# Kernel tuning notes

Hardware: AMD Instinct MI355X
Metric: run time of the kernel (lower is better)

Reference implementation:

```python
import jax, jax.numpy as jnp
import numpy as np

B, S, H = 1, 2048, 1024      # batch, seq, hidden_size
E, I, K = 32, 768, 4         # num_experts, moe_intermediate_size, top_k
NORM_TOPK = True


def setup_inputs() -> dict:
    key = jax.random.key(0)
    k0, k1, k2, k3, k4 = jax.random.split(key, 5)
    sc = 0.02  # typical init std
    return {
        "hidden_states": jax.random.normal(k0, (B, S, H), dtype=jnp.float32),
        "router_w": jax.random.normal(k1, (E, H), dtype=jnp.float32) * sc,
        "gate_w":   jax.random.normal(k2, (E, I, H), dtype=jnp.float32) * sc,
        "up_w":     jax.random.normal(k3, (E, I, H), dtype=jnp.float32) * sc,
        "down_w":   jax.random.normal(k4, (E, H, I), dtype=jnp.float32) * sc,
    }


def _moe(hidden_states, router_w, gate_w, up_w, down_w):
    b, s, h = hidden_states.shape
    x = hidden_states.reshape(-1, h)                       # [T, H]
    # --- router: linear -> fp32 softmax -> top-k -> renorm ---
    logits = x @ router_w.T                                # [T, E]
    probs = jax.nn.softmax(logits.astype(jnp.float32), axis=-1)
    vals, idx = jax.lax.top_k(probs, K)                    # [T, K]
    if NORM_TOPK:
        vals = vals / jnp.sum(vals, axis=-1, keepdims=True)
    vals = vals.astype(x.dtype)
    # dense combine weights [T, E]: zero for unselected experts
    combine = jnp.sum(jax.nn.one_hot(idx, probs.shape[-1], dtype=x.dtype)
                      * vals[..., None], axis=1)           # [T, E]
    # --- per-expert gated-SiLU MLP, weighted combine (scan over experts) ---
    def step(acc, ws):
        wg, wu, wd, we = ws                                # [I,H],[I,H],[H,I],[T]
        hidden = jax.nn.silu(x @ wg.T) * (x @ wu.T)        # [T, I]
        return acc + we[:, None] * (hidden @ wd.T), None
    acc0 = jnp.zeros_like(x)
    out, _ = jax.lax.scan(step, acc0, (gate_w, up_w, down_w, combine.T))
    return out.reshape(b, s, h)


def reference(hidden_states, router_w, gate_w, up_w, down_w):
    return _moe(hidden_states, router_w, gate_w, up_w, down_w)
```

## Files before the change

kernel.cpp:

```cpp
#include <hip/hip_runtime.h>
#include <hip/hip_bf16.h>

typedef __attribute__((ext_vector_type(8))) short short8;
typedef __attribute__((ext_vector_type(4))) float f32x4;

#define T_TOK 2048
#define H_DIM 1024
#define E_NUM 32
#define I_DIM 768
#define TOPK  4
#define NPAIR (T_TOK*TOPK)

#define OFF_IDX     0
#define OFF_TKW     (32*1024)
#define OFF_COUNTS  (64*1024)
#define OFF_OFFSETS (65*1024)
#define OFF_CURSORS (66*1024)
#define OFF_PERM    (68*1024)
#define OFF_PAIRW   (100*1024)
#define OFF_POS     (132*1024)
#define OFF_XBF     (1024*1024)
#define OFF_H       (6*1024*1024)
#define OFF_Y       (20*1024*1024)

__device__ __forceinline__ unsigned short f2bf(float f) {
    __hip_bfloat16 b = __float2bfloat16(f);
    unsigned short u;
    __builtin_memcpy(&u, &b, 2);
    return u;
}
__device__ __forceinline__ unsigned int pk2(float lo, float hi) {
    return (unsigned int)f2bf(lo) | ((unsigned int)f2bf(hi) << 16);
}

__global__ __launch_bounds__(256)
void k_xcvt(const float* __restrict__ x, unsigned short* __restrict__ xbf)
{
    int g = blockIdx.x * 256 + threadIdx.x;
    const float4* p = (const float4*)(x + (size_t)g * 8);
    float4 a = p[0], b = p[1];
    uint4 o = { pk2(a.x,a.y), pk2(a.z,a.w), pk2(b.x,b.y), pk2(b.z,b.w) };
    *(uint4*)(xbf + (size_t)g * 8) = o;
}

__global__ __launch_bounds__(64)
void k_router(const float* __restrict__ x, const float* __restrict__ rw,
              int* __restrict__ idx, float* __restrict__ tkw, int* __restrict__ counts)
{
    int t = blockIdx.x;
    int lane = threadIdx.x;
    const float4* xr = (const float4*)(x + (size_t)t * H_DIM);
    float4 xv[4];
#pragma unroll
    for (int m = 0; m < 4; ++m) xv[m] = xr[m * 64 + lane];

    __shared__ float logits[E_NUM];
    for (int e = 0; e < E_NUM; ++e) {
        const float4* wr = (const float4*)(rw + (size_t)e * H_DIM);
        float acc = 0.f;
#pragma unroll
        for (int m = 0; m < 4; ++m) {
            float4 wv = wr[m * 64 + lane];
            acc += xv[m].x * wv.x + xv[m].y * wv.y + xv[m].z * wv.z + xv[m].w * wv.w;
        }
#pragma unroll
        for (int s = 32; s > 0; s >>= 1) acc += __shfl_xor(acc, s);
        if (lane == 0) logits[e] = acc;
    }
    __syncthreads();
    if (lane == 0) {
        float m = -1e30f;
        for (int e = 0; e < E_NUM; ++e) m = fmaxf(m, logits[e]);
        for (int e = 0; e < E_NUM; ++e) logits[e] = expf(logits[e] - m);
        float vals[TOPK]; int ids[TOPK]; float s = 0.f;
        for (int k = 0; k < TOPK; ++k) {
            float bv = -1.f; int be = 0;
            for (int e = 0; e < E_NUM; ++e)
                if (logits[e] > bv) { bv = logits[e]; be = e; }
            vals[k] = bv; ids[k] = be; logits[be] = -2.f; s += bv;
        }
        float invs = 1.f / s;
        for (int k = 0; k < TOPK; ++k) {
            idx[t * TOPK + k] = ids[k];
            tkw[t * TOPK + k] = vals[k] * invs;
            atomicAdd(&counts[ids[k]], 1);
        }
    }
}

__global__ void k_scan(const int* __restrict__ counts, int* __restrict__ offsets,
                       int* __restrict__ cursors)
{
    if (threadIdx.x == 0) {
        int acc = 0;
        for (int e = 0; e < E_NUM; ++e) { offsets[e] = acc; cursors[e] = acc; acc += counts[e]; }
        offsets[E_NUM] = acc;
    }
}

__global__ __launch_bounds__(256)
void k_scatter(const int* __restrict__ idx, const float* __restrict__ tkw,
               int* __restrict__ cursors, int* __restrict__ perm,
               float* __restrict__ pairw, int* __restrict__ pos)
{
    int g = blockIdx.x * 256 + threadIdx.x;
    if (g >= NPAIR) return;
    int e = idx[g];
    int p = atomicAdd(&cursors[e], 1);
    perm[p] = g >> 2;
    pairw[p] = tkw[g];
    pos[g] = p;
}

#define GU_BN 64
#define GU_BM 256
#define GU_BK 64
#define PAD   72

__global__ __launch_bounds__(256, 2)
void k_gateup(const unsigned short* __restrict__ xbf, const float* __restrict__ gw,
              const float* __restrict__ uw, const int* __restrict__ offsets,
              const int* __restrict__ perm, unsigned short* __restrict__ h)
{
    int e  = blockIdx.z;
    int r0 = offsets[e], r1 = offsets[e + 1];
    int row0 = r0 + blockIdx.y * GU_BM;
    if (row0 >= r1) return;
    int nrows = min(GU_BM, r1 - row0);
    int ib = blockIdx.x * GU_BN;

    __shared__ __align__(16) unsigned short As[GU_BM * PAD];
    __shared__ __align__(16) unsigned short Bgs[GU_BN * PAD];
    __shared__ __align__(16) unsigned short Bus[GU_BN * PAD];
    __shared__ int rtok[GU_BM];

    int tid = threadIdx.x;
    rtok[tid] = perm[min(row0 + tid, r1 - 1)];

    const float* wgb = gw + ((size_t)e * I_DIM + ib) * H_DIM;
    const float* wub = uw + ((size_t)e * I_DIM + ib) * H_DIM;

    int w = tid >> 6;
    int lane = tid & 63;
    int l15 = lane & 15, lhi = lane >> 4;

    f32x4 accg[4][4], accu[4][4];
#pragma unroll
    for (int a = 0; a < 4; ++a)
#pragma unroll
        for (int b = 0; b < 4; ++b) { accg[a][b] = 0.f; accu[a][b] = 0.f; }

    for (int kb = 0; kb < H_DIM; kb += GU_BK) {
        __syncthreads();
#pragma unroll
        for (int p = 0; p < 8; ++p) {
            int q = tid + p * 256;
            int row = q >> 3, kg = q & 7;
            uint4 v = *(const uint4*)(xbf + (size_t)rtok[row] * H_DIM + kb + kg * 8);
            *(uint4*)&As[row * PAD + kg * 8] = v;
        }
#pragma unroll
        for (int p = 0; p < 2; ++p) {
            int q = tid + p * 256;
            int row = q >> 3, kg = q & 7;
            const float* sg = wgb + (size_t)row * H_DIM + kb + kg * 8;
            float4 a0 = *(const float4*)sg, a1 = *(const float4*)(sg + 4);
            uint4 vg = { pk2(a0.x,a0.y), pk2(a0.z,a0.w), pk2(a1.x,a1.y), pk2(a1.z,a1.w) };
            *(uint4*)&Bgs[row * PAD + kg * 8] = vg;
            const float* su = wub + (size_t)row * H_DIM + kb + kg * 8;
            float4 b0 = *(const float4*)su, b1 = *(const float4*)(su + 4);
            uint4 vu = { pk2(b0.x,b0.y), pk2(b0.z,b0.w), pk2(b1.x,b1.y), pk2(b1.z,b1.w) };
            *(uint4*)&Bus[row * PAD + kg * 8] = vu;
        }
        __syncthreads();
#pragma unroll
        for (int kk = 0; kk < 2; ++kk) {
            short8 av[4], bgv[4], buv[4];
            int ko = kk * 32 + lhi * 8;
#pragma unroll
            for (int f = 0; f < 4; ++f) {
                av[f]  = *(const short8*)&As[(w * 64 + f * 16 + l15) * PAD + ko];
                bgv[f] = *(const short8*)&Bgs[(f * 16 + l15) * PAD + ko];
                buv[f] = *(const short8*)&Bus[(f * 16 + l15) * PAD + ko];
            }
#pragma unroll
            for (int fm = 0; fm < 4; ++fm)
#pragma unroll
                for (int fn = 0; fn < 4; ++fn) {
                    accg[fm][fn] = __builtin_amdgcn_mfma_f32_16x16x32_bf16(av[fm], bgv[fn], accg[fm][fn], 0, 0, 0);
                    accu[fm][fn] = __builtin_amdgcn_mfma_f32_16x16x32_bf16(av[fm], buv[fn], accu[fm][fn], 0, 0, 0);
                }
        }
    }
#pragma unroll
    for (int fm = 0; fm < 4; ++fm) {
#pragma unroll
        for (int j = 0; j < 4; ++j) {
            int r = w * 64 + fm * 16 + lhi * 4 + j;
            if (r < nrows) {
                size_t orow = (size_t)(row0 + r) * I_DIM + ib + l15;
#pragma unroll
                for (int fn = 0; fn < 4; ++fn) {
                    float g = accg[fm][fn][j];
                    float u = accu[fm][fn][j];
                    float hv = (g / (1.f + __expf(-g))) * u;
                    h[orow + fn * 16] = f2bf(hv);
                }
            }
        }
    }
}

#define DN_BN 64
#define DN_BM 256
#define DN_BK 64

__global__ __launch_bounds__(256, 2)
void k_down(const float* __restrict__ dw, const int* __restrict__ offsets,
            const float* __restrict__ pairw, const unsigned short* __restrict__ h,
            float* __restrict__ y)
{
    int e  = blockIdx.z;
    int r0 = offsets[e], r1 = offsets[e + 1];
    int row0 = r0 + blockIdx.y * DN_BM;
    if (row0 >= r1) return;
    int nrows = min(DN_BM, r1 - row0);
    int cb = blockIdx.x * DN_BN;

    __shared__ __align__(16) unsigned short As[DN_BM * PAD];
    __shared__ __align__(16) unsigned short Bs[DN_BN * PAD];
    __shared__ float pw[DN_BM];

    int tid = threadIdx.x;
    pw[tid] = pairw[min(row0 + tid, r1 - 1)];

    const float* wdb = dw + ((size_t)e * H_DIM + cb) * I_DIM;
    int w = tid >> 6, lane = tid & 63;
    int l15 = lane & 15, lhi = lane >> 4;

    f32x4 acc[4][4];
#pragma unroll
    for (int a = 0; a < 4; ++a)
#pragma unroll
        for (int b = 0; b < 4; ++b) acc[a][b] = 0.f;

    for (int kb = 0; kb < I_DIM; kb += DN_BK) {
        __syncthreads();
#pragma unroll
        for (int p = 0; p < 8; ++p) {
            int q = tid + p * 256;
            int row = q >> 3, kg = q & 7;
            int rr = min(row0 + row, r1 - 1);
            uint4 v = *(const uint4*)(h + (size_t)rr * I_DIM + kb + kg * 8);
            *(uint4*)&As[row * PAD + kg * 8] = v;
        }
#pragma unroll
        for (int p = 0; p < 2; ++p) {
            int q = tid + p * 256;
            int row = q >> 3, kg = q & 7;
            const float* sd = wdb + (size_t)row * I_DIM + kb + kg * 8;
            float4 a0 = *(const float4*)sd, a1 = *(const float4*)(sd + 4);
            uint4 vd = { pk2(a0.x,a0.y), pk2(a0.z,a0.w), pk2(a1.x,a1.y), pk2(a1.z,a1.w) };
            *(uint4*)&Bs[row * PAD + kg * 8] = vd;
        }
        __syncthreads();
#pragma unroll
        for (int kk = 0; kk < 2; ++kk) {
            short8 av[4], bv[4];
            int ko = kk * 32 + lhi * 8;
#pragma unroll
            for (int f = 0; f < 4; ++f) {
                av[f] = *(const short8*)&As[(w * 64 + f * 16 + l15) * PAD + ko];
                bv[f] = *(const short8*)&Bs[(f * 16 + l15) * PAD + ko];
            }
#pragma unroll
            for (int fm = 0; fm < 4; ++fm)
#pragma unroll
                for (int fn = 0; fn < 4; ++fn)
                    acc[fm][fn] = __builtin_amdgcn_mfma_f32_16x16x32_bf16(av[fm], bv[fn], acc[fm][fn], 0, 0, 0);
        }
    }
#pragma unroll
    for (int fm = 0; fm < 4; ++fm) {
#pragma unroll
        for (int j = 0; j < 4; ++j) {
            int r = w * 64 + fm * 16 + lhi * 4 + j;
            if (r < nrows) {
                float s = pw[r];
                size_t orow = (size_t)(row0 + r) * H_DIM + cb + l15;
#pragma unroll
                for (int fn = 0; fn < 4; ++fn)
                    y[orow + fn * 16] = s * acc[fm][fn][j];
            }
        }
    }
}

__global__ __launch_bounds__(256)
void k_combine(const float* __restrict__ y, const int* __restrict__ pos,
               float* __restrict__ out)
{
    int g = blockIdx.x * 256 + threadIdx.x;
    int t = g >> 10;
    int hc = g & 1023;
    const int* pp = pos + t * TOPK;
    float s = y[(size_t)pp[0] * H_DIM + hc] + y[(size_t)pp[1] * H_DIM + hc]
            + y[(size_t)pp[2] * H_DIM + hc] + y[(size_t)pp[3] * H_DIM + hc];
    out[g] = s;
}

extern "C" void kernel_launch(void* const* d_in, const int* in_sizes, int n_in,
                              void* d_out, int out_size, void* d_ws, size_t ws_size,
                              hipStream_t stream)
{
    const float* x  = (const float*)d_in[0];
    const float* rw = (const float*)d_in[1];
    const float* gw = (const float*)d_in[2];
    const float* uw = (const float*)d_in[3];
    const float* dw = (const float*)d_in[4];
    float* out = (float*)d_out;

    char* ws = (char*)d_ws;
    int*   idx     = (int*)  (ws + OFF_IDX);
    float* tkw     = (float*)(ws + OFF_TKW);
    int*   counts  = (int*)  (ws + OFF_COUNTS);
    int*   offsets = (int*)  (ws + OFF_OFFSETS);
    int*   cursors = (int*)  (ws + OFF_CURSORS);
    int*   perm    = (int*)  (ws + OFF_PERM);
    float* pairw   = (float*)(ws + OFF_PAIRW);
    int*   pos     = (int*)  (ws + OFF_POS);
    unsigned short* xbf = (unsigned short*)(ws + OFF_XBF);
    unsigned short* h   = (unsigned short*)(ws + OFF_H);
    float* y            = (float*)(ws + OFF_Y);

    hipMemsetAsync(counts, 0, E_NUM * sizeof(int), stream);

    k_xcvt<<<T_TOK * H_DIM / (256 * 8), 256, 0, stream>>>(x, xbf);
    k_router<<<T_TOK, 64, 0, stream>>>(x, rw, idx, tkw, counts);
    k_scan<<<1, 64, 0, stream>>>(counts, offsets, cursors);
    k_scatter<<<(NPAIR + 255) / 256, 256, 0, stream>>>(idx, tkw, cursors, perm, pairw, pos);

    dim3 g3(I_DIM / GU_BN, NPAIR / GU_BM, E_NUM);
    k_gateup<<<g3, 256, 0, stream>>>(xbf, gw, uw, offsets, perm, h);

    dim3 g4(H_DIM / DN_BN, NPAIR / DN_BM, E_NUM);
    k_down<<<g4, 256, 0, stream>>>(dw, offsets, pairw, h, y);

    k_combine<<<T_TOK * H_DIM / 256, 256, 0, stream>>>(y, pos, out);
}
```

Measured before the change: 479.2 us.

## Register-prefetch next K tile in gate/up and down GEMMs

Both expert GEMM kernels now load the next K tile from global memory into registers while MFMAs run on the current shared-memory tile, then write those registers to LDS after a barrier. Token and row indices are hoisted into per-thread registers so they are not recomputed each iteration. This is meant to hide global load latency behind compute. The cost is higher register pressure: roughly 32 VGPRs for the A prefetch plus weight staging, on top of 128 accumulator values in gate/up. That could hurt occupancy under launch_bounds(256,2) or cause spills.

```diff
diff --git a/kernel.cpp b/kernel.cpp
--- a/kernel.cpp
+++ b/kernel.cpp
@@ -116,6 +116,7 @@
 #define GU_BM 256
 #define GU_BK 64
 #define PAD   72
+#define GU_NT (H_DIM / GU_BK)
 
 __global__ __launch_bounds__(256, 2)
 void k_gateup(const unsigned short* __restrict__ xbf, const float* __restrict__ gw,
@@ -136,6 +137,12 @@
 
     int tid = threadIdx.x;
     rtok[tid] = perm[min(row0 + tid, r1 - 1)];
+    __syncthreads();
+
+    int mytok[8];
+#pragma unroll
+    for (int p = 0; p < 8; ++p) mytok[p] = rtok[(tid + p * 256) >> 3];
+    int akg = tid & 7;
 
     const float* wgb = gw + ((size_t)e * I_DIM + ib) * H_DIM;
     const float* wub = uw + ((size_t)e * I_DIM + ib) * H_DIM;
@@ -150,29 +157,44 @@
 #pragma unroll
         for (int b = 0; b < 4; ++b) { accg[a][b] = 0.f; accu[a][b] = 0.f; }
 
-    for (int kb = 0; kb < H_DIM; kb += GU_BK) {
+    uint4 pa[8];
+    float4 pg0[2], pg1[2], pu0[2], pu1[2];
+
+#define GU_LOAD(KB) do {                                                          \
+    _Pragma("unroll")                                                             \
+    for (int p = 0; p < 8; ++p)                                                   \
+        pa[p] = *(const uint4*)(xbf + (size_t)mytok[p] * H_DIM + (KB) + akg * 8); \
+    _Pragma("unroll")                                                             \
+    for (int it = 0; it < 2; ++it) {                                              \
+        int q = tid + it * 256; int brow = q >> 3, bkg = q & 7;                   \
+        const float* sg = wgb + (size_t)brow * H_DIM + (KB) + bkg * 8;            \
+        pg0[it] = *(const float4*)sg; pg1[it] = *(const float4*)(sg + 4);         \
+        const float* su = wub + (size_t)brow * H_DIM + (KB) + bkg * 8;            \
+        pu0[it] = *(const float4*)su; pu1[it] = *(const float4*)(su + 4);         \
+    } } while (0)
+
+#define GU_WRITE() do {                                                           \
+    _Pragma("unroll")                                                             \
+    for (int p = 0; p < 8; ++p) {                                                 \
+        int arow = (tid + p * 256) >> 3;                                          \
+        *(uint4*)&As[arow * PAD + akg * 8] = pa[p];                               \
+    }                                                                             \
+    _Pragma("unroll")                                                             \
+    for (int it = 0; it < 2; ++it) {                                              \
+        int q = tid + it * 256; int brow = q >> 3, bkg = q & 7;                   \
+        uint4 vg = { pk2(pg0[it].x,pg0[it].y), pk2(pg0[it].z,pg0[it].w),          \
+                     pk2(pg1[it].x,pg1[it].y), pk2(pg1[it].z,pg1[it].w) };        \
+        *(uint4*)&Bgs[brow * PAD + bkg * 8] = vg;                                 \
+        uint4 vu = { pk2(pu0[it].x,pu0[it].y), pk2(pu0[it].z,pu0[it].w),          \
+                     pk2(pu1[it].x,pu1[it].y), pk2(pu1[it].z,pu1[it].w) };        \
+        *(uint4*)&Bus[brow * PAD + bkg * 8] = vu;                                 \
+    } } while (0)
+
+    GU_LOAD(0);
+    for (int kt = 0; kt < GU_NT; ++kt) {
+        GU_WRITE();
         __syncthreads();
-#pragma unroll
-        for (int p = 0; p < 8; ++p) {
-            int q = tid + p * 256;
-            int row = q >> 3, kg = q & 7;
-            uint4 v = *(const uint4*)(xbf + (size_t)rtok[row] * H_DIM + kb + kg * 8);
-            *(uint4*)&As[row * PAD + kg * 8] = v;
-        }
-#pragma unroll
-        for (int p = 0; p < 2; ++p) {
-            int q = tid + p * 256;
-            int row = q >> 3, kg = q & 7;
-            const float* sg = wgb + (size_t)row * H_DIM + kb + kg * 8;
-            float4 a0 = *(const float4*)sg, a1 = *(const float4*)(sg + 4);
-            uint4 vg = { pk2(a0.x,a0.y), pk2(a0.z,a0.w), pk2(a1.x,a1.y), pk2(a1.z,a1.w) };
-            *(uint4*)&Bgs[row * PAD + kg * 8] = vg;
-            const float* su = wub + (size_t)row * H_DIM + kb + kg * 8;
-            float4 b0 = *(const float4*)su, b1 = *(const float4*)(su + 4);
-            uint4 vu = { pk2(b0.x,b0.y), pk2(b0.z,b0.w), pk2(b1.x,b1.y), pk2(b1.z,b1.w) };
-            *(uint4*)&Bus[row * PAD + kg * 8] = vu;
-        }
-        __syncthreads();
+        if (kt + 1 < GU_NT) GU_LOAD((kt + 1) * GU_BK);
 #pragma unroll
         for (int kk = 0; kk < 2; ++kk) {
             short8 av[4], bgv[4], buv[4];
@@ -191,6 +213,7 @@
                     accu[fm][fn] = __builtin_amdgcn_mfma_f32_16x16x32_bf16(av[fm], buv[fn], accu[fm][fn], 0, 0, 0);
                 }
         }
+        __syncthreads();
     }
 #pragma unroll
     for (int fm = 0; fm < 4; ++fm) {
@@ -214,6 +237,7 @@
 #define DN_BN 64
 #define DN_BM 256
 #define DN_BK 64
+#define DN_NT (I_DIM / DN_BK)
 
 __global__ __launch_bounds__(256, 2)
 void k_down(const float* __restrict__ dw, const int* __restrict__ offsets,
@@ -233,6 +257,15 @@
 
     int tid = threadIdx.x;
     pw[tid] = pairw[min(row0 + tid, r1 - 1)];
+    __syncthreads();
+
+    size_t myar[8];
+#pragma unroll
+    for (int p = 0; p < 8; ++p) {
+        int rr = min(row0 + ((tid + p * 256) >> 3), r1 - 1);
+        myar[p] = (size_t)rr * I_DIM;
+    }
+    int akg = tid & 7;
 
     const float* wdb = dw + ((size_t)e * H_DIM + cb) * I_DIM;
     int w = tid >> 6, lane = tid & 63;
@@ -244,26 +277,39 @@
 #pragma unroll
         for (int b = 0; b < 4; ++b) acc[a][b] = 0.f;
 
-    for (int kb = 0; kb < I_DIM; kb += DN_BK) {
+    uint4 pa[8];
+    float4 pd0[2], pd1[2];
+
+#define DN_LOAD(KB) do {                                                     \
+    _Pragma("unroll")                                                        \
+    for (int p = 0; p < 8; ++p)                                              \
+        pa[p] = *(const uint4*)(h + myar[p] + (KB) + akg * 8);               \
+    _Pragma("unroll")                                                        \
+    for (int it = 0; it < 2; ++it) {                                         \
+        int q = tid + it * 256; int brow = q >> 3, bkg = q & 7;              \
+        const float* sd = wdb + (size_t)brow * I_DIM + (KB) + bkg * 8;       \
+        pd0[it] = *(const float4*)sd; pd1[it] = *(const float4*)(sd + 4);    \
+    } } while (0)
+
+#define DN_WRITE() do {                                                      \
+    _Pragma("unroll")                                                        \
+    for (int p = 0; p < 8; ++p) {                                            \
+        int arow = (tid + p * 256) >> 3;                                     \
+        *(uint4*)&As[arow * PAD + akg * 8] = pa[p];                          \
+    }                                                                        \
+    _Pragma("unroll")                                                        \
+    for (int it = 0; it < 2; ++it) {                                         \
+        int q = tid + it * 256; int brow = q >> 3, bkg = q & 7;              \
+        uint4 vd = { pk2(pd0[it].x,pd0[it].y), pk2(pd0[it].z,pd0[it].w),     \
+                     pk2(pd1[it].x,pd1[it].y), pk2(pd1[it].z,pd1[it].w) };   \
+        *(uint4*)&Bs[brow * PAD + bkg * 8] = vd;                             \
+    } } while (0)
+
+    DN_LOAD(0);
+    for (int kt = 0; kt < DN_NT; ++kt) {
+        DN_WRITE();
         __syncthreads();
-#pragma unroll
-        for (int p = 0; p < 8; ++p) {
-            int q = tid + p * 256;
-            int row = q >> 3, kg = q & 7;
-            int rr = min(row0 + row, r1 - 1);
-            uint4 v = *(const uint4*)(h + (size_t)rr * I_DIM + kb + kg * 8);
-            *(uint4*)&As[row * PAD + kg * 8] = v;
-        }
-#pragma unroll
-        for (int p = 0; p < 2; ++p) {
-            int q = tid + p * 256;
-            int row = q >> 3, kg = q & 7;
-            const float* sd = wdb + (size_t)row * I_DIM + kb + kg * 8;
-            float4 a0 = *(const float4*)sd, a1 = *(const float4*)(sd + 4);
-            uint4 vd = { pk2(a0.x,a0.y), pk2(a0.z,a0.w), pk2(a1.x,a1.y), pk2(a1.z,a1.w) };
-            *(uint4*)&Bs[row * PAD + kg * 8] = vd;
-        }
-        __syncthreads();
+        if (kt + 1 < DN_NT) DN_LOAD((kt + 1) * DN_BK);
 #pragma unroll
         for (int kk = 0; kk < 2; ++kk) {
             short8 av[4], bv[4];
@@ -279,6 +325,7 @@
                 for (int fn = 0; fn < 4; ++fn)
                     acc[fm][fn] = __builtin_amdgcn_mfma_f32_16x16x32_bf16(av[fm], bv[fn], acc[fm][fn], 0, 0, 0);
         }
+        __syncthreads();
     }
 #pragma unroll
     for (int fm = 0; fm < 4; ++fm) {
```

Result: slower. 661.6 us (+38.1%).

## Give each wave private weight tiles and read activations directly from global

Applied to the files above, without the earlier changes.

In the gate/up and down expert GEMMs, the shared A tile and the block-wide __syncthreads are removed. Each wavefront now stages its own private copy of the bf16-converted weight tile in LDS and loads its activation rows straight from global memory into registers. The aim is to drop block barriers and the A-tile LDS round trip. In exchange, every wave repeats the fp32 weight loads and bf16 conversion (four times per block), and gate/up needs about 74KB of dynamic LDS. That LDS size may cut occupancy and could exceed the default dynamic shared limit.

```diff
diff --git a/kernel.cpp b/kernel.cpp
--- a/kernel.cpp
+++ b/kernel.cpp
@@ -116,6 +116,8 @@
 #define GU_BM 256
 #define GU_BK 64
 #define PAD   72
+#define GU_NT (H_DIM / GU_BK)
+#define WB    (GU_BN * PAD)
 
 __global__ __launch_bounds__(256, 2)
 void k_gateup(const unsigned short* __restrict__ xbf, const float* __restrict__ gw,
@@ -129,20 +131,24 @@
     int nrows = min(GU_BM, r1 - row0);
     int ib = blockIdx.x * GU_BN;
 
-    __shared__ __align__(16) unsigned short As[GU_BM * PAD];
-    __shared__ __align__(16) unsigned short Bgs[GU_BN * PAD];
-    __shared__ __align__(16) unsigned short Bus[GU_BN * PAD];
-    __shared__ int rtok[GU_BM];
-
-    int tid = threadIdx.x;
-    rtok[tid] = perm[min(row0 + tid, r1 - 1)];
+    extern __shared__ __align__(16) unsigned short smem[];
+    int tid = threadIdx.x, w = tid >> 6, lane = tid & 63;
+    unsigned short* bg = smem + (size_t)w * (2 * WB);
+    unsigned short* bu = bg + WB;
+    int l15 = lane & 15, lhi = lane >> 4;
+
+    size_t arow[4];
+#pragma unroll
+    for (int fm = 0; fm < 4; ++fm) {
+        int r = w * 64 + fm * 16 + l15;
+        arow[fm] = (size_t)perm[min(row0 + r, r1 - 1)] * H_DIM;
+    }
 
     const float* wgb = gw + ((size_t)e * I_DIM + ib) * H_DIM;
     const float* wub = uw + ((size_t)e * I_DIM + ib) * H_DIM;
 
-    int w = tid >> 6;
-    int lane = tid & 63;
-    int l15 = lane & 15, lhi = lane >> 4;
+    int srow = lane >> 3;
+    int sc   = (lane & 7) * 8;
 
     f32x4 accg[4][4], accu[4][4];
 #pragma unroll
@@ -150,47 +156,47 @@
 #pragma unroll
         for (int b = 0; b < 4; ++b) { accg[a][b] = 0.f; accu[a][b] = 0.f; }
 
-    for (int kb = 0; kb < H_DIM; kb += GU_BK) {
-        __syncthreads();
-#pragma unroll
-        for (int p = 0; p < 8; ++p) {
-            int q = tid + p * 256;
-            int row = q >> 3, kg = q & 7;
-            uint4 v = *(const uint4*)(xbf + (size_t)rtok[row] * H_DIM + kb + kg * 8);
-            *(uint4*)&As[row * PAD + kg * 8] = v;
-        }
-#pragma unroll
-        for (int p = 0; p < 2; ++p) {
-            int q = tid + p * 256;
-            int row = q >> 3, kg = q & 7;
-            const float* sg = wgb + (size_t)row * H_DIM + kb + kg * 8;
-            float4 a0 = *(const float4*)sg, a1 = *(const float4*)(sg + 4);
-            uint4 vg = { pk2(a0.x,a0.y), pk2(a0.z,a0.w), pk2(a1.x,a1.y), pk2(a1.z,a1.w) };
-            *(uint4*)&Bgs[row * PAD + kg * 8] = vg;
-            const float* su = wub + (size_t)row * H_DIM + kb + kg * 8;
-            float4 b0 = *(const float4*)su, b1 = *(const float4*)(su + 4);
-            uint4 vu = { pk2(b0.x,b0.y), pk2(b0.z,b0.w), pk2(b1.x,b1.y), pk2(b1.z,b1.w) };
-            *(uint4*)&Bus[row * PAD + kg * 8] = vu;
-        }
-        __syncthreads();
+#define GU_STAGE(KB) do {                                                              \
+    _Pragma("unroll 4")                                                                \
+    for (int rr = 0; rr < 8; ++rr) {                                                   \
+        int row = rr * 8 + srow;                                                       \
+        const float* sg = wgb + (size_t)row * H_DIM + (KB) + sc;                       \
+        float4 g0 = *(const float4*)sg, g1 = *(const float4*)(sg + 4);                 \
+        const float* su = wub + (size_t)row * H_DIM + (KB) + sc;                       \
+        float4 u0 = *(const float4*)su, u1 = *(const float4*)(su + 4);                 \
+        uint4 vg = { pk2(g0.x,g0.y), pk2(g0.z,g0.w), pk2(g1.x,g1.y), pk2(g1.z,g1.w) }; \
+        *(uint4*)&bg[row * PAD + sc] = vg;                                             \
+        uint4 vu = { pk2(u0.x,u0.y), pk2(u0.z,u0.w), pk2(u1.x,u1.y), pk2(u1.z,u1.w) }; \
+        *(uint4*)&bu[row * PAD + sc] = vu;                                             \
+    } } while (0)
+
+    GU_STAGE(0);
+    for (int kt = 0; kt < GU_NT; ++kt) {
+        int kb = kt * GU_BK;
+        short8 av[4][2];
+#pragma unroll
+        for (int fm = 0; fm < 4; ++fm)
+#pragma unroll
+            for (int kk = 0; kk < 2; ++kk)
+                av[fm][kk] = *(const short8*)(xbf + arow[fm] + kb + kk * 32 + lhi * 8);
 #pragma unroll
         for (int kk = 0; kk < 2; ++kk) {
-            short8 av[4], bgv[4], buv[4];
+            short8 bgv[4], buv[4];
             int ko = kk * 32 + lhi * 8;
 #pragma unroll
             for (int f = 0; f < 4; ++f) {
-                av[f]  = *(const short8*)&As[(w * 64 + f * 16 + l15) * PAD + ko];
-                bgv[f] = *(const short8*)&Bgs[(f * 16 + l15) * PAD + ko];
-                buv[f] = *(const short8*)&Bus[(f * 16 + l15) * PAD + ko];
+                bgv[f] = *(const short8*)&bg[(f * 16 + l15) * PAD + ko];
+                buv[f] = *(const short8*)&bu[(f * 16 + l15) * PAD + ko];
             }
 #pragma unroll
             for (int fm = 0; fm < 4; ++fm)
 #pragma unroll
                 for (int fn = 0; fn < 4; ++fn) {
-                    accg[fm][fn] = __builtin_amdgcn_mfma_f32_16x16x32_bf16(av[fm], bgv[fn], accg[fm][fn], 0, 0, 0);
-                    accu[fm][fn] = __builtin_amdgcn_mfma_f32_16x16x32_bf16(av[fm], buv[fn], accu[fm][fn], 0, 0, 0);
+                    accg[fm][fn] = __builtin_amdgcn_mfma_f32_16x16x32_bf16(av[fm][kk], bgv[fn], accg[fm][fn], 0, 0, 0);
+                    accu[fm][fn] = __builtin_amdgcn_mfma_f32_16x16x32_bf16(av[fm][kk], buv[fn], accu[fm][fn], 0, 0, 0);
                 }
         }
+        if (kt + 1 < GU_NT) GU_STAGE(kb + GU_BK);
     }
 #pragma unroll
     for (int fm = 0; fm < 4; ++fm) {
@@ -214,6 +220,8 @@
 #define DN_BN 64
 #define DN_BM 256
 #define DN_BK 64
+#define DN_NT (I_DIM / DN_BK)
+#define WBD   (DN_BN * PAD)
 
 __global__ __launch_bounds__(256, 2)
 void k_down(const float* __restrict__ dw, const int* __restrict__ offsets,
@@ -227,16 +235,21 @@
     int nrows = min(DN_BM, r1 - row0);
     int cb = blockIdx.x * DN_BN;
 
-    __shared__ __align__(16) unsigned short As[DN_BM * PAD];
-    __shared__ __align__(16) unsigned short Bs[DN_BN * PAD];
-    __shared__ float pw[DN_BM];
-
-    int tid = threadIdx.x;
-    pw[tid] = pairw[min(row0 + tid, r1 - 1)];
+    __shared__ __align__(16) unsigned short smemd[4 * WBD];
+    int tid = threadIdx.x, w = tid >> 6, lane = tid & 63;
+    unsigned short* bd = smemd + (size_t)w * WBD;
+    int l15 = lane & 15, lhi = lane >> 4;
+
+    size_t arow[4];
+#pragma unroll
+    for (int fm = 0; fm < 4; ++fm) {
+        int r = w * 64 + fm * 16 + l15;
+        arow[fm] = (size_t)min(row0 + r, r1 - 1) * I_DIM;
+    }
 
     const float* wdb = dw + ((size_t)e * H_DIM + cb) * I_DIM;
-    int w = tid >> 6, lane = tid & 63;
-    int l15 = lane & 15, lhi = lane >> 4;
+    int srow = lane >> 3;
+    int sc   = (lane & 7) * 8;
 
     f32x4 acc[4][4];
 #pragma unroll
@@ -244,41 +257,39 @@
 #pragma unroll
         for (int b = 0; b < 4; ++b) acc[a][b] = 0.f;
 
-    for (int kb = 0; kb < I_DIM; kb += DN_BK) {
-        __syncthreads();
-#pragma unroll
-        for (int p = 0; p < 8; ++p) {
-            int q = tid + p * 256;
-            int row = q >> 3, kg = q & 7;
-            int rr = min(row0 + row, r1 - 1);
-            uint4 v = *(const uint4*)(h + (size_t)rr * I_DIM + kb + kg * 8);
-            *(uint4*)&As[row * PAD + kg * 8] = v;
-        }
-#pragma unroll
-        for (int p = 0; p < 2; ++p) {
-            int q = tid + p * 256;
-            int row = q >> 3, kg = q & 7;
-            const float* sd = wdb + (size_t)row * I_DIM + kb + kg * 8;
-            float4 a0 = *(const float4*)sd, a1 = *(const float4*)(sd + 4);
-            uint4 vd = { pk2(a0.x,a0.y), pk2(a0.z,a0.w), pk2(a1.x,a1.y), pk2(a1.z,a1.w) };
-            *(uint4*)&Bs[row * PAD + kg * 8] = vd;
-        }
-        __syncthreads();
+#define DN_STAGE(KB) do {                                                              \
+    _Pragma("unroll 4")                                                                \
+    for (int rr = 0; rr < 8; ++rr) {                                                   \
+        int row = rr * 8 + srow;                                                       \
+        const float* sd = wdb + (size_t)row * I_DIM + (KB) + sc;                       \
+        float4 d0 = *(const float4*)sd, d1 = *(const float4*)(sd + 4);                 \
+        uint4 vd = { pk2(d0.x,d0.y), pk2(d0.z,d0.w), pk2(d1.x,d1.y), pk2(d1.z,d1.w) }; \
+        *(uint4*)&bd[row * PAD + sc] = vd;                                             \
+    } } while (0)
+
+    DN_STAGE(0);
+    for (int kt = 0; kt < DN_NT; ++kt) {
+        int kb = kt * DN_BK;
+        short8 av[4][2];
+#pragma unroll
+        for (int fm = 0; fm < 4; ++fm)
+#pragma unroll
+            for (int kk = 0; kk < 2; ++kk)
+                av[fm][kk] = *(const short8*)(h + arow[fm] + kb + kk * 32 + lhi * 8);
 #pragma unroll
         for (int kk = 0; kk < 2; ++kk) {
-            short8 av[4], bv[4];
+            short8 bv[4];
             int ko = kk * 32 + lhi * 8;
 #pragma unroll
-            for (int f = 0; f < 4; ++f) {
-                av[f] = *(const short8*)&As[(w * 64 + f * 16 + l15) * PAD + ko];
-                bv[f] = *(const short8*)&Bs[(f * 16 + l15) * PAD + ko];
-            }
+            for (int f = 0; f < 4; ++f)
+                bv[f] = *(const short8*)&bd[(f * 16 + l15) * PAD + ko];
 #pragma unroll
             for (int fm = 0; fm < 4; ++fm)
 #pragma unroll
                 for (int fn = 0; fn < 4; ++fn)
-                    acc[fm][fn] = __builtin_amdgcn_mfma_f32_16x16x32_bf16(av[fm], bv[fn], acc[fm][fn], 0, 0, 0);
-        }
+                    acc[fm][fn] = __builtin_amdgcn_mfma_f32_16x16x32_bf16(av[fm][kk], bv[fn], acc[fm][fn], 0, 0, 0);
+        }
+        if (kt + 1 < DN_NT) DN_STAGE(kb + DN_BK);
     }
 #pragma unroll
     for (int fm = 0; fm < 4; ++fm) {
@@ -286,7 +297,7 @@
         for (int j = 0; j < 4; ++j) {
             int r = w * 64 + fm * 16 + lhi * 4 + j;
             if (r < nrows) {
-                float s = pw[r];
+                float s = pairw[row0 + r];
                 size_t orow = (size_t)(row0 + r) * H_DIM + cb + l15;
 #pragma unroll
                 for (int fn = 0; fn < 4; ++fn)
@@ -341,7 +352,7 @@
     k_scatter<<<(NPAIR + 255) / 256, 256, 0, stream>>>(idx, tkw, cursors, perm, pairw, pos);
 
     dim3 g3(I_DIM / GU_BN, NPAIR / GU_BM, E_NUM);
-    k_gateup<<<g3, 256, 0, stream>>>(xbf, gw, uw, offsets, perm, h);
+    k_gateup<<<g3, 256, 4 * 2 * WB * sizeof(unsigned short), stream>>>(xbf, gw, uw, offsets, perm, h);
 
     dim3 g4(H_DIM / DN_BN, NPAIR / DN_BM, E_NUM);
     k_down<<<g4, 256, 0, stream>>>(dw, offsets, pairw, h, y);
```

Result: slower. 629.9 us (+31.5%).

## Fuse top-k combine into down-proj via atomics and halve GEMM row tiles

Applied to the files above, without the earlier changes.

Removes the separate combine kernel and the intermediate y buffer. The down-projection epilogue now atomically adds weighted results straight into the zeroed output at each token's row, and the output is cleared with a memset. Row tiles of both the gate/up and down GEMMs shrink from 256 to 128 with a higher occupancy hint, and per-thread row addresses are hoisted out of the k loop. The trade-off is 8M float atomics, nondeterministic summation order, and the fp32 weights being reloaded by twice as many row blocks.

```diff
diff --git a/kernel.cpp b/kernel.cpp
--- a/kernel.cpp
+++ b/kernel.cpp
@@ -18,10 +18,8 @@
 #define OFF_CURSORS (66*1024)
 #define OFF_PERM    (68*1024)
 #define OFF_PAIRW   (100*1024)
-#define OFF_POS     (132*1024)
 #define OFF_XBF     (1024*1024)
 #define OFF_H       (6*1024*1024)
-#define OFF_Y       (20*1024*1024)
 
 __device__ __forceinline__ unsigned short f2bf(float f) {
     __hip_bfloat16 b = __float2bfloat16(f);
@@ -101,7 +99,7 @@
 __global__ __launch_bounds__(256)
 void k_scatter(const int* __restrict__ idx, const float* __restrict__ tkw,
                int* __restrict__ cursors, int* __restrict__ perm,
-               float* __restrict__ pairw, int* __restrict__ pos)
+               float* __restrict__ pairw)
 {
     int g = blockIdx.x * 256 + threadIdx.x;
     if (g >= NPAIR) return;
@@ -109,15 +107,15 @@
     int p = atomicAdd(&cursors[e], 1);
     perm[p] = g >> 2;
     pairw[p] = tkw[g];
-    pos[g] = p;
 }
 
 #define GU_BN 64
-#define GU_BM 256
+#define GU_BM 128
 #define GU_BK 64
 #define PAD   72
-
-__global__ __launch_bounds__(256, 2)
+#define GU_NT (H_DIM / GU_BK)
+
+__global__ __launch_bounds__(256, 3)
 void k_gateup(const unsigned short* __restrict__ xbf, const float* __restrict__ gw,
               const float* __restrict__ uw, const int* __restrict__ offsets,
               const int* __restrict__ perm, unsigned short* __restrict__ h)
@@ -135,7 +133,13 @@
     __shared__ int rtok[GU_BM];
 
     int tid = threadIdx.x;
-    rtok[tid] = perm[min(row0 + tid, r1 - 1)];
+    if (tid < GU_BM) rtok[tid] = perm[min(row0 + tid, r1 - 1)];
+    __syncthreads();
+
+    int mytok[4];
+#pragma unroll
+    for (int p = 0; p < 4; ++p) mytok[p] = rtok[(tid + p * 256) >> 3];
+    int akg = tid & 7;
 
     const float* wgb = gw + ((size_t)e * I_DIM + ib) * H_DIM;
     const float* wub = uw + ((size_t)e * I_DIM + ib) * H_DIM;
@@ -144,20 +148,20 @@
     int lane = tid & 63;
     int l15 = lane & 15, lhi = lane >> 4;
 
-    f32x4 accg[4][4], accu[4][4];
-#pragma unroll
-    for (int a = 0; a < 4; ++a)
+    f32x4 accg[2][4], accu[2][4];
+#pragma unroll
+    for (int a = 0; a < 2; ++a)
 #pragma unroll
         for (int b = 0; b < 4; ++b) { accg[a][b] = 0.f; accu[a][b] = 0.f; }
 
     for (int kb = 0; kb < H_DIM; kb += GU_BK) {
         __syncthreads();
 #pragma unroll
-        for (int p = 0; p < 8; ++p) {
+        for (int p = 0; p < 4; ++p) {
             int q = tid + p * 256;
-            int row = q >> 3, kg = q & 7;
-            uint4 v = *(const uint4*)(xbf + (size_t)rtok[row] * H_DIM + kb + kg * 8);
-            *(uint4*)&As[row * PAD + kg * 8] = v;
+            int row = q >> 3;
+            uint4 v = *(const uint4*)(xbf + (size_t)mytok[p] * H_DIM + kb + akg * 8);
+            *(uint4*)&As[row * PAD + akg * 8] = v;
         }
 #pragma unroll
         for (int p = 0; p < 2; ++p) {
@@ -175,16 +179,18 @@
         __syncthreads();
 #pragma unroll
         for (int kk = 0; kk < 2; ++kk) {
-            short8 av[4], bgv[4], buv[4];
+            short8 av[2], bgv[4], buv[4];
             int ko = kk * 32 + lhi * 8;
 #pragma unroll
+            for (int f = 0; f < 2; ++f)
+                av[f]  = *(const short8*)&As[(w * 32 + f * 16 + l15) * PAD + ko];
+#pragma unroll
             for (int f = 0; f < 4; ++f) {
-                av[f]  = *(const short8*)&As[(w * 64 + f * 16 + l15) * PAD + ko];
                 bgv[f] = *(const short8*)&Bgs[(f * 16 + l15) * PAD + ko];
                 buv[f] = *(const short8*)&Bus[(f * 16 + l15) * PAD + ko];
             }
 #pragma unroll
-            for (int fm = 0; fm < 4; ++fm)
+            for (int fm = 0; fm < 2; ++fm)
 #pragma unroll
                 for (int fn = 0; fn < 4; ++fn) {
                     accg[fm][fn] = __builtin_amdgcn_mfma_f32_16x16x32_bf16(av[fm], bgv[fn], accg[fm][fn], 0, 0, 0);
@@ -193,10 +199,10 @@
         }
     }
 #pragma unroll
-    for (int fm = 0; fm < 4; ++fm) {
+    for (int fm = 0; fm < 2; ++fm) {
 #pragma unroll
         for (int j = 0; j < 4; ++j) {
-            int r = w * 64 + fm * 16 + lhi * 4 + j;
+            int r = w * 32 + fm * 16 + lhi * 4 + j;
             if (r < nrows) {
                 size_t orow = (size_t)(row0 + r) * I_DIM + ib + l15;
 #pragma unroll
@@ -212,13 +218,14 @@
 }
 
 #define DN_BN 64
-#define DN_BM 256
+#define DN_BM 128
 #define DN_BK 64
-
-__global__ __launch_bounds__(256, 2)
+#define DN_NT (I_DIM / DN_BK)
+
+__global__ __launch_bounds__(256, 3)
 void k_down(const float* __restrict__ dw, const int* __restrict__ offsets,
-            const float* __restrict__ pairw, const unsigned short* __restrict__ h,
-            float* __restrict__ y)
+            const float* __restrict__ pairw, const int* __restrict__ perm,
+            const unsigned short* __restrict__ h, float* __restrict__ out)
 {
     int e  = blockIdx.z;
     int r0 = offsets[e], r1 = offsets[e + 1];
@@ -230,29 +237,42 @@
     __shared__ __align__(16) unsigned short As[DN_BM * PAD];
     __shared__ __align__(16) unsigned short Bs[DN_BN * PAD];
     __shared__ float pw[DN_BM];
+    __shared__ int   ptok[DN_BM];
 
     int tid = threadIdx.x;
-    pw[tid] = pairw[min(row0 + tid, r1 - 1)];
+    if (tid < DN_BM) {
+        int rr = min(row0 + tid, r1 - 1);
+        pw[tid]   = pairw[rr];
+        ptok[tid] = perm[rr];
+    }
+    __syncthreads();
+
+    size_t myar[4];
+#pragma unroll
+    for (int p = 0; p < 4; ++p) {
+        int rr = min(row0 + ((tid + p * 256) >> 3), r1 - 1);
+        myar[p] = (size_t)rr * I_DIM;
+    }
+    int akg = tid & 7;
 
     const float* wdb = dw + ((size_t)e * H_DIM + cb) * I_DIM;
     int w = tid >> 6, lane = tid & 63;
     int l15 = lane & 15, lhi = lane >> 4;
 
-    f32x4 acc[4][4];
-#pragma unroll
-    for (int a = 0; a < 4; ++a)
+    f32x4 acc[2][4];
+#pragma unroll
+    for (int a = 0; a < 2; ++a)
 #pragma unroll
         for (int b = 0; b < 4; ++b) acc[a][b] = 0.f;
 
     for (int kb = 0; kb < I_DIM; kb += DN_BK) {
         __syncthreads();
 #pragma unroll
-        for (int p = 0; p < 8; ++p) {
+        for (int p = 0; p < 4; ++p) {
             int q = tid + p * 256;
-            int row = q >> 3, kg = q & 7;
-            int rr = min(row0 + row, r1 - 1);
-            uint4 v = *(const uint4*)(h + (size_t)rr * I_DIM + kb + kg * 8);
-            *(uint4*)&As[row * PAD + kg * 8] = v;
+            int row = q >> 3;
+            uint4 v = *(const uint4*)(h + myar[p] + kb + akg * 8);
+            *(uint4*)&As[row * PAD + akg * 8] = v;
         }
 #pragma unroll
         for (int p = 0; p < 2; ++p) {
@@ -266,47 +286,35 @@
         __syncthreads();
 #pragma unroll
         for (int kk = 0; kk < 2; ++kk) {
-            short8 av[4], bv[4];
+            short8 av[2], bv[4];
             int ko = kk * 32 + lhi * 8;
 #pragma unroll
-            for (int f = 0; f < 4; ++f) {
-                av[f] = *(const short8*)&As[(w * 64 + f * 16 + l15) * PAD + ko];
+            for (int f = 0; f < 2; ++f)
+                av[f] = *(const short8*)&As[(w * 32 + f * 16 + l15) * PAD + ko];
+#pragma unroll
+            for (int f = 0; f < 4; ++f)
                 bv[f] = *(const short8*)&Bs[(f * 16 + l15) * PAD + ko];
-            }
-#pragma unroll
-            for (int fm = 0; fm < 4; ++fm)
+#pragma unroll
+            for (int fm = 0; fm < 2; ++fm)
 #pragma unroll
                 for (int fn = 0; fn < 4; ++fn)
                     acc[fm][fn] = __builtin_amdgcn_mfma_f32_16x16x32_bf16(av[fm], bv[fn], acc[fm][fn], 0, 0, 0);
         }
     }
 #pragma unroll
-    for (int fm = 0; fm < 4; ++fm) {
+    for (int fm = 0; fm < 2; ++fm) {
 #pragma unroll
         for (int j = 0; j < 4; ++j) {
-            int r = w * 64 + fm * 16 + lhi * 4 + j;
+            int r = w * 32 + fm * 16 + lhi * 4 + j;
             if (r < nrows) {
                 float s = pw[r];
-                size_t orow = (size_t)(row0 + r) * H_DIM + cb + l15;
+                float* obase = out + (size_t)ptok[r] * H_DIM + cb + l15;
 #pragma unroll
                 for (int fn = 0; fn < 4; ++fn)
-                    y[orow + fn * 16] = s * acc[fm][fn][j];
+                    atomicAdd(obase + fn * 16, s * acc[fm][fn][j]);
             }
         }
     }
-}
-
-__global__ __launch_bounds__(256)
-void k_combine(const float* __restrict__ y, const int* __restrict__ pos,
-               float* __restrict__ out)
-{
-    int g = blockIdx.x * 256 + threadIdx.x;
-    int t = g >> 10;
-    int hc = g & 1023;
-    const int* pp = pos + t * TOPK;
-    float s = y[(size_t)pp[0] * H_DIM + hc] + y[(size_t)pp[1] * H_DIM + hc]
-            + y[(size_t)pp[2] * H_DIM + hc] + y[(size_t)pp[3] * H_DIM + hc];
-    out[g] = s;
 }
 
 extern "C" void kernel_launch(void* const* d_in, const int* in_sizes, int n_in,
@@ -328,23 +336,20 @@
     int*   cursors = (int*)  (ws + OFF_CURSORS);
     int*   perm    = (int*)  (ws + OFF_PERM);
     float* pairw   = (float*)(ws + OFF_PAIRW);
-    int*   pos     = (int*)  (ws + OFF_POS);
     unsigned short* xbf = (unsigned short*)(ws + OFF_XBF);
     unsigned short* h   = (unsigned short*)(ws + OFF_H);
-    float* y            = (float*)(ws + OFF_Y);
 
     hipMemsetAsync(counts, 0, E_NUM * sizeof(int), stream);
+    hipMemsetAsync(out, 0, (size_t)T_TOK * H_DIM * sizeof(float), stream);
 
     k_xcvt<<<T_TOK * H_DIM / (256 * 8), 256, 0, stream>>>(x, xbf);
     k_router<<<T_TOK, 64, 0, stream>>>(x, rw, idx, tkw, counts);
     k_scan<<<1, 64, 0, stream>>>(counts, offsets, cursors);
-    k_scatter<<<(NPAIR + 255) / 256, 256, 0, stream>>>(idx, tkw, cursors, perm, pairw, pos);
+    k_scatter<<<(NPAIR + 255) / 256, 256, 0, stream>>>(idx, tkw, cursors, perm, pairw);
 
     dim3 g3(I_DIM / GU_BN, NPAIR / GU_BM, E_NUM);
     k_gateup<<<g3, 256, 0, stream>>>(xbf, gw, uw, offsets, perm, h);
 
     dim3 g4(H_DIM / DN_BN, NPAIR / DN_BM, E_NUM);
-    k_down<<<g4, 256, 0, stream>>>(dw, offsets, pairw, h, y);
-
-    k_combine<<<T_TOK * H_DIM / 256, 256, 0, stream>>>(y, pos, out);
-}
+    k_down<<<g4, 256, 0, stream>>>(dw, offsets, pairw, perm, h, out);
+}
```

After: 498.8 us. 4.1% more time.
